# Optimization experiments

Hardware: AMD Instinct MI355X
Metric: run time of the kernel (lower is better)

Reference implementation:

```python
import jax, jax.numpy as jnp
import numpy as np

N = 100000       # nodes
E = 1600000      # edges
NFEAT = 128
NHID = 128
NCLASS = 64
NHEAD = 4
NLAYER = 3
LRELU_ALPHA = 0.2


def setup_inputs() -> dict:
    key = jax.random.key(0)
    ks = jax.random.split(key, 7)
    x = jax.random.normal(ks[0], (N, NFEAT), jnp.float32)
    edge_index = jax.random.randint(ks[1], (2, E), 0, N, jnp.int32)
    # xavier-uniform-ish init scales (gain for relu baked into scale roughly)
    Win = jax.random.normal(ks[2], (NFEAT, NHID), jnp.float32) * (2.0 / (NFEAT + NHID)) ** 0.5
    b_in = jnp.zeros((NHID,), jnp.float32)
    # per hidden layer, per head: a split into (src, dst) halves of the (1, 2*in) vector
    a_hid = jax.random.normal(ks[3], (NLAYER - 1, NHEAD, 2, NHID), jnp.float32) * 0.1
    W_hid = jax.random.normal(ks[4], (NLAYER - 1, NHEAD, NHID, NHID // NHEAD), jnp.float32) * (2.0 / (NHID + NHID // NHEAD)) ** 0.5
    a_out = jax.random.normal(ks[5], (2, NHID), jnp.float32) * 0.1
    W_out = jax.random.normal(ks[6], (NHID, NCLASS), jnp.float32) * (2.0 / (NHID + NCLASS)) ** 0.5
    return dict(x=x, edge_index=edge_index, Win=Win, b_in=b_in,
                a_hid=a_hid, W_hid=W_hid, a_out=a_out, W_out=W_out)


def _segment_softmax(logits, seg, n):
    # numerically stable softmax over groups defined by seg (axis 0)
    m = jax.ops.segment_max(logits, seg, num_segments=n)
    e = jnp.exp(logits - m[seg])
    s = jax.ops.segment_sum(e, seg, num_segments=n)
    return e / s[seg]


def _gat_conv(h, row, col, a, W):
    # h: [N, D]; a: [H, 2, D]; W: [H, D, Dh]
    n = h.shape[0]
    H = a.shape[0]
    s_src = h @ a[:, 0, :].T  # [N, H]
    s_dst = h @ a[:, 1, :].T  # [N, H]
    logits = jax.nn.leaky_relu(s_src[row] + s_dst[col], LRELU_ALPHA)  # [E, H]
    alpha = _segment_softmax(logits, row, n)  # softmax grouped by row (edge_index[0])
    h_col = h[col]  # [E, D] gathered once, reused per head
    outs = []
    for hd in range(H):  # small fixed head loop keeps peak memory at [E, D]
        agg = jax.ops.segment_sum(alpha[:, hd, None] * h_col, row, num_segments=n)  # [N, D]
        outs.append(agg @ W[hd])  # weight applied AFTER aggregation, as in source
    return jnp.concatenate(outs, axis=1)


def reference(x, edge_index, Win, b_in, a_hid, W_hid, a_out, W_out):
    row, col = edge_index[0], edge_index[1]
    h = jax.nn.elu(x @ Win + b_in)  # in_linear + ELU (dropout is identity in eval/p=0)
    for l in range(a_hid.shape[0]):
        h = jax.nn.elu(_gat_conv(h, row, col, a_hid[l], W_hid[l]))
    # final conv: single head to nclass, no activation
    return _gat_conv(h, row, col, a_out[None], W_out[None])
```

## Files before the change

kernel.cpp:

```cpp
#include <hip/hip_runtime.h>
#include <hip/hip_bf16.h>
#include <cstdint>
#include <cstddef>

#define LRELU_ALPHA 0.2f
#define LOG2E 1.44269504088896f

typedef __attribute__((ext_vector_type(8))) short short8;
typedef __attribute__((ext_vector_type(4))) float f32x4;
typedef _Float16 h2v __attribute__((ext_vector_type(2)));

__device__ __forceinline__ unsigned short f2bf(float f) {
    unsigned int u = __float_as_uint(f);
    unsigned int r = (u + 0x7fffu + ((u >> 16) & 1u)) >> 16;
    return (unsigned short)r;
}
__device__ __forceinline__ float bf2f(unsigned int lo16) {
    return __uint_as_float(lo16 << 16);
}
__device__ __forceinline__ unsigned int pk2(float a, float b) {
    return (unsigned int)f2bf(a) | ((unsigned int)f2bf(b) << 16);
}
__device__ __forceinline__ float fexp2(float x) {
#if __has_builtin(__builtin_amdgcn_exp2f)
    return __builtin_amdgcn_exp2f(x);
#else
    return __expf(x * 0.69314718056f);
#endif
}
__device__ __forceinline__ h2v pkrtz(float a, float b) {
#if __has_builtin(__builtin_amdgcn_cvt_pkrtz)
    auto r = __builtin_amdgcn_cvt_pkrtz(a, b);
    union { decltype(r) i; h2v o; } u;
    u.i = r;
    return u.o;
#else
    h2v r; r.x = (_Float16)a; r.y = (_Float16)b; return r;
#endif
}
__device__ __forceinline__ unsigned int pack_lo(unsigned int a, unsigned int b) {
#if __has_builtin(__builtin_amdgcn_perm)
    return __builtin_amdgcn_perm(a, b, 0x01000504u);
#else
    return (a & 0xffffu) | (b << 16);
#endif
}
__device__ __forceinline__ unsigned int pack_hi(unsigned int a, unsigned int b) {
#if __has_builtin(__builtin_amdgcn_perm)
    return __builtin_amdgcn_perm(a, b, 0x03020706u);
#else
    return (a >> 16) | (b & 0xffff0000u);
#endif
}
union U32H2 { unsigned int u; h2v h; };
__device__ __forceinline__ float dot2f(unsigned int a, h2v w, float acc) {
    U32H2 c; c.u = a;
#if __has_builtin(__builtin_amdgcn_fdot2)
    return __builtin_amdgcn_fdot2(c.h, w, acc, false);
#else
    return acc + (float)c.h.x * (float)w.x + (float)c.h.y * (float)w.y;
#endif
}


__global__ void hist8_k(const int* __restrict__ ei, int* __restrict__ counts8,
                        int* __restrict__ rank,
                        float* __restrict__ sdA, float* __restrict__ sdB,
                        float* __restrict__ sdC, unsigned int* __restrict__ hW,
                        int N_, int E_) {
    int rep = blockIdx.x & 7;
    int base = (blockIdx.x * 256 + threadIdx.x) * 8;
    int* cnt = counts8 + (size_t)rep * N_;
    if (base + 8 <= E_) {
        int4 a = *(const int4*)&ei[base];
        int4 b = *(const int4*)&ei[base + 4];
        int rk[8];
        rk[0] = atomicAdd(&cnt[a.x], 1);
        rk[1] = atomicAdd(&cnt[a.y], 1);
        rk[2] = atomicAdd(&cnt[a.z], 1);
        rk[3] = atomicAdd(&cnt[a.w], 1);
        rk[4] = atomicAdd(&cnt[b.x], 1);
        rk[5] = atomicAdd(&cnt[b.y], 1);
        rk[6] = atomicAdd(&cnt[b.z], 1);
        rk[7] = atomicAdd(&cnt[b.w], 1);
        *(int4*)&rank[base]     = make_int4(rk[0], rk[1], rk[2], rk[3]);
        *(int4*)&rank[base + 4] = make_int4(rk[4], rk[5], rk[6], rk[7]);
    } else if (base < E_) {
        for (int j = 0; j < 8 && base + j < E_; j++)
            rank[base + j] = atomicAdd(&cnt[ei[base + j]], 1);
    }
    if (blockIdx.x == 0) {
        int t = threadIdx.x;
        if (t < 4) { sdA[N_ * 4 + t] = -1e30f; sdB[N_ * 4 + t] = -1e30f; }
        if (t == 4) sdC[N_] = -1e30f;
        if (t >= 32 && t < 64)  hW[(size_t)N_ * 32 + (t - 32)] = 0u;
        if (t >= 64 && t < 128) hW[(size_t)N_ * 64 + (t - 64)] = 0u;
    }
}

__global__ void scan_block_k(const int* __restrict__ counts8, int* __restrict__ tmp,
                             int* __restrict__ bsum, int n) {
    __shared__ int s[256];
    int i = blockIdx.x * 256 + threadIdx.x;
    int v = 0;
    if (i < n) {
        int c = 0;
        #pragma unroll
        for (int r = 0; r < 8; r++) c += counts8[(size_t)r * n + i];
        v = (c + 7) & ~7;
    }
    s[threadIdx.x] = v;
    __syncthreads();
    for (int d = 1; d < 256; d <<= 1) {
        int t_ = (threadIdx.x >= d) ? s[threadIdx.x - d] : 0;
        __syncthreads();
        s[threadIdx.x] += t_;
        __syncthreads();
    }
    if (i < n) tmp[i] = s[threadIdx.x];
    if (threadIdx.x == 255) bsum[blockIdx.x] = s[255];
}

__global__ void scan_sums_k(int* bsum, int nb) {
    __shared__ int s[512];
    int v = ((int)threadIdx.x < nb) ? bsum[threadIdx.x] : 0;
    s[threadIdx.x] = v;
    __syncthreads();
    for (int d = 1; d < 512; d <<= 1) {
        int t_ = ((int)threadIdx.x >= d) ? s[threadIdx.x - d] : 0;
        __syncthreads();
        s[threadIdx.x] += t_;
        __syncthreads();
    }
    if ((int)threadIdx.x < nb) bsum[threadIdx.x] = s[threadIdx.x] - v;
}

__global__ void finalize_k(const int* __restrict__ tmp, const int* __restrict__ bsum,
                           const int* __restrict__ counts8, int* __restrict__ base8,
                           int* __restrict__ off, int* __restrict__ scol, int N_, int n) {
    int i = blockIdx.x * 256 + threadIdx.x;
    if (i < n) {
        int end = tmp[i] + bsum[blockIdx.x];
        off[i + 1] = end;
        int c[8], cnt = 0;
        #pragma unroll
        for (int r = 0; r < 8; r++) { c[r] = counts8[(size_t)r * n + i]; cnt += c[r]; }
        int padded = (cnt + 7) & ~7;
        int pos = end - padded;
        #pragma unroll
        for (int r = 0; r < 8; r++) { base8[(size_t)r * n + i] = pos; pos += c[r]; }
        for (; pos < end; pos++) scol[pos] = N_;
    }
    if (i == 0) off[0] = 0;
}

__global__ void scatter8_k(const int* __restrict__ ei, const int* __restrict__ rank,
                           const int* __restrict__ base8, int* __restrict__ scol,
                           int N_, int E_) {
    int rep = blockIdx.x & 7;
    int base = (blockIdx.x * 256 + threadIdx.x) * 8;
    const int* cb = base8 + (size_t)rep * N_;
    if (base + 8 <= E_) {
        int4 a   = *(const int4*)&ei[base];
        int4 b   = *(const int4*)&ei[base + 4];
        int4 ra  = *(const int4*)&rank[base];
        int4 rb  = *(const int4*)&rank[base + 4];
        int4 ca  = *(const int4*)&ei[E_ + base];
        int4 cb4 = *(const int4*)&ei[E_ + base + 4];
        scol[cb[a.x] + ra.x] = ca.x;
        scol[cb[a.y] + ra.y] = ca.y;
        scol[cb[a.z] + ra.z] = ca.z;
        scol[cb[a.w] + ra.w] = ca.w;
        scol[cb[b.x] + rb.x] = cb4.x;
        scol[cb[b.y] + rb.y] = cb4.y;
        scol[cb[b.z] + rb.z] = cb4.z;
        scol[cb[b.w] + rb.w] = cb4.w;
    } else if (base < E_) {
        for (int j = 0; j < 8 && base + j < E_; j++) {
            int r = ei[base + j];
            scol[cb[r] + rank[base + j]] = ei[E_ + base + j];
        }
    }
}


__global__ void repack_all(const float* __restrict__ Win, const float* __restrict__ Whid,
                           const float* __restrict__ ahid, const float* __restrict__ Wout,
                           const float* __restrict__ aout,
                           unsigned short* __restrict__ W0, unsigned short* __restrict__ W1,
                           unsigned short* __restrict__ W2, unsigned short* __restrict__ W3) {
    int i = blockIdx.x * 256 + threadIdx.x;
    if (i < 16384) {
        int n = i >> 7, k = i & 127;
        W0[i] = f2bf(Win[k * 128 + n]);
    } else if (i < 16384 + 2 * 18432) {
        int j = i - 16384;
        int l = j / 18432;
        int jj = j - l * 18432;
        int n = jj >> 7, k = jj & 127;
        float v;
        if (n < 128) {
            int hd = n >> 5, c = n & 31;
            v = Whid[(size_t)l * 16384 + (hd * 128 + k) * 32 + c];
        } else if (n < 136) {
            int ch = n - 128;
            v = ahid[((size_t)l * 8 + ch) * 128 + k] * LOG2E;
        } else {
            v = 0.f;
        }
        (l ? W2 : W1)[jj] = f2bf(v);
    } else if (i < 16384 + 2 * 18432 + 10240) {
        int j = i - (16384 + 2 * 18432);
        int n = j >> 7, k = j & 127;
        float v;
        if (n < 64)       v = Wout[k * 64 + n];
        else if (n < 66)  v = aout[(n - 64) * 128 + k] * LOG2E;
        else              v = 0.f;
        W3[j] = f2bf(v);
    }
}


template <int KJ, int KJA, bool ELU_ACT, bool BIAS, int OUTM, bool ABF16, int SC_H>
__global__ __launch_bounds__(256) void gemm_mfma(const void* __restrict__ Xv,
                                                 const unsigned short* __restrict__ WT,
                                                 const float* __restrict__ bias,
                                                 void* __restrict__ Yv,
                                                 float* __restrict__ ssn,
                                                 float* __restrict__ sdn, int nRows) {
    constexpr int NT = KJA / 16;
    constexpr int NTS = KJ / 16;
    constexpr int WS = 136;
    __shared__ unsigned short sWT[KJA * WS];
    int t = threadIdx.x;
    for (int i = t; i < KJA * 16; i += 256) {
        int n = i >> 4, k8 = i & 15;
        uint4 v = *(const uint4*)&WT[n * 128 + k8 * 8];
        *(uint4*)&sWT[n * WS + k8 * 8] = v;
    }
    __syncthreads();

    int lane = t & 63;
    int wv = t >> 6;
    int m0 = blockIdx.x * 128 + wv * 32;
    int l16 = lane & 15;
    int q4 = lane >> 4;

    short8 afr[4][2];
    #pragma unroll
    for (int rt = 0; rt < 2; rt++) {
        int row = m0 + rt * 16 + l16;
        bool vr = row < nRows;
        if (ABF16) {
            const unsigned int* xp = (const unsigned int*)Xv + (size_t)row * 64 + q4 * 4;
            #pragma unroll
            for (int kk = 0; kk < 4; kk++) {
                uint4 u = make_uint4(0u, 0u, 0u, 0u);
                if (vr) u = *(const uint4*)(xp + kk * 16);
                afr[kk][rt] = *(short8*)&u;
            }
        } else {
            const float* xp = (const float*)Xv + (size_t)row * 128 + q4 * 8;
            #pragma unroll
            for (int kk = 0; kk < 4; kk++) {
                float4 a0 = make_float4(0.f, 0.f, 0.f, 0.f), a1 = a0;
                if (vr) {
                    a0 = *(const float4*)(xp + kk * 32);
                    a1 = *(const float4*)(xp + kk * 32 + 4);
                }
                unsigned int u[4];
                u[0] = pk2(a0.x, a0.y); u[1] = pk2(a0.z, a0.w);
                u[2] = pk2(a1.x, a1.y); u[3] = pk2(a1.z, a1.w);
                afr[kk][rt] = *(short8*)u;
            }
        }
    }

    f32x4 acc[2][NT] = {};
    #pragma unroll
    for (int kk = 0; kk < 4; kk++) {
        #pragma unroll
        for (int ct = 0; ct < NT; ct++) {
            int n = ct * 16 + l16;
            short8 bf = *(const short8*)&sWT[n * WS + kk * 32 + q4 * 8];
            #pragma unroll
            for (int rt = 0; rt < 2; rt++)
                acc[rt][ct] = __builtin_amdgcn_mfma_f32_16x16x32_bf16(afr[kk][rt], bf, acc[rt][ct], 0, 0, 0);
        }
    }

    #pragma unroll
    for (int rt = 0; rt < 2; rt++) {
        #pragma unroll
        for (int q = 0; q < 4; q++) {
            int row = m0 + rt * 16 + q4 * 4 + q;
            if (row >= nRows) continue;
            #pragma unroll
            for (int ct = 0; ct < NTS; ct++) {
                int colc = ct * 16 + l16;
                float v = acc[rt][ct][q];
                if (BIAS) v += bias[colc];
                if (ELU_ACT) v = v > 0.f ? v : (__expf(v) - 1.f);
                if (OUTM == 1) {
                    ((unsigned short*)Yv)[(size_t)row * KJ + colc] = f2bf(v);
                } else if (OUTM == 2) {
                    union { _Float16 hf; unsigned short us; } cv;
                    cv.hf = (_Float16)v;
                    ((unsigned short*)Yv)[(size_t)row * KJ + colc] = cv.us;
                } else {
                    ((float*)Yv)[(size_t)row * KJ + colc] = v;
                }
            }
            if (SC_H > 0) {
                if (l16 < 2 * SC_H) {
                    float v = acc[rt][NT - 1][q];
                    float* dst = (l16 & 1) ? sdn : ssn;
                    dst[row * SC_H + (l16 >> 1)] = v;
                }
            }
        }
    }
}


template <int DHT, int H, bool ELU_ACT, bool BF16O>
__global__ __launch_bounds__(256) void edge_agg_v(const unsigned int* __restrict__ hW2,
                                                  const float* __restrict__ ssrc,
                                                  const float* __restrict__ sdst,
                                                  const int* __restrict__ off,
                                                  const int* __restrict__ scol,
                                                  void* __restrict__ outv, int nRows) {
    constexpr int FPL = DHT / 16;
    constexpr int UPL = FPL / 2;
    int lane = threadIdx.x & 63;
    int sub = lane & 15;
    int g = lane >> 4;
    int wv = threadIdx.x >> 6;
    int r = __builtin_amdgcn_readfirstlane(blockIdx.x * 4 + wv);
    if (r >= nRows) return;
    int begin = off[r], end = off[r + 1];

    int head = (H == 4) ? (sub >> 2) : 0;
    float ssl = ssrc[r * H + head];

    float acc[FPL] = {};
    float den = 0.f;

    for (int i = begin; i < end; i += 8) {
        int2 cc = *(const int2*)&scol[i + 2 * g];
        int cA = cc.x, cB = cc.y;
        float sdA = sdst[cA * H + head];
        float sdB = sdst[cB * H + head];
        unsigned int hA[UPL], hB[UPL];
        int oA = cA * (DHT / 2) + sub * UPL;
        int oB = cB * (DHT / 2) + sub * UPL;
        if (UPL == 4) {
            *(uint4*)hA = *(const uint4*)&hW2[oA];
            *(uint4*)hB = *(const uint4*)&hW2[oB];
        } else {
            *(uint2*)hA = *(const uint2*)&hW2[oA];
            *(uint2*)hB = *(const uint2*)&hW2[oB];
        }
        float lgA = ssl + sdA;
        float wA = fexp2(fmaxf(lgA, LRELU_ALPHA * lgA));
        float lgB = ssl + sdB;
        float wB = fexp2(fmaxf(lgB, LRELU_ALPHA * lgB));
        den += wA + wB;
        h2v w2 = pkrtz(wA, wB);
        #pragma unroll
        for (int q = 0; q < UPL; q++) {
            acc[2 * q]     = dot2f(pack_lo(hA[q], hB[q]), w2, acc[2 * q]);
            acc[2 * q + 1] = dot2f(pack_hi(hA[q], hB[q]), w2, acc[2 * q + 1]);
        }
    }

    #pragma unroll
    for (int s = 16; s < 64; s <<= 1) {
        den += __shfl_xor(den, s);
        #pragma unroll
        for (int p = 0; p < FPL; p++) acc[p] += __shfl_xor(acc[p], s);
    }
    float inv = den > 0.f ? 1.f / den : 0.f;

    float v[FPL];
    #pragma unroll
    for (int p = 0; p < FPL; p++) {
        float tv = acc[p] * inv;
        if (ELU_ACT) tv = tv > 0.f ? tv : (__expf(tv) - 1.f);
        v[p] = tv;
    }

    if (DHT == 128) {
        if (BF16O)
            ((unsigned int*)outv)[(size_t)r * 64 + sub * 4 + g] = pk2(v[2 * g], v[2 * g + 1]);
        else
            *(float2*)&((float*)outv)[(size_t)r * 128 + sub * 8 + 2 * g] =
                make_float2(v[2 * g], v[2 * g + 1]);
    } else {
        ((float*)outv)[(size_t)r * DHT + sub * FPL + g] = v[g];
    }
}


extern "C" void kernel_launch(void* const* d_in, const int* in_sizes, int n_in,
                              void* d_out, int out_size, void* d_ws, size_t ws_size,
                              hipStream_t stream) {
    const float* x    = (const float*)d_in[0];
    const int*   ei   = (const int*)d_in[1];
    const float* Win  = (const float*)d_in[2];
    const float* bin  = (const float*)d_in[3];
    const float* ahid = (const float*)d_in[4];
    const float* Whid = (const float*)d_in[5];
    const float* aout = (const float*)d_in[6];
    const float* Wout = (const float*)d_in[7];
    float* out = (float*)d_out;

    const int N_ = in_sizes[0] / 128;
    const int E_ = in_sizes[1] / 2;

    char* p = (char*)d_ws;
    auto alloc = [&](size_t bytes) {
        char* q = p;
        p += (bytes + 511) & ~(size_t)511;
        return q;
    };
    int* counts8 = (int*)alloc((size_t)N_ * 8 * 4);
    int* base8   = (int*)alloc((size_t)N_ * 8 * 4);
    int* rank    = (int*)alloc((size_t)(E_ + 8) * 4);
    int* tmp     = (int*)alloc((size_t)N_ * 4);
    int* off     = (int*)alloc((size_t)(N_ + 1) * 4);
    int* bsum    = (int*)alloc(4096);
    int* scol    = (int*)alloc((size_t)(E_ + 8 * N_ + 64) * 4);
    float* ssrcA = (float*)alloc((size_t)(N_ + 1) * 4 * 4);
    float* sdstA = (float*)alloc((size_t)(N_ + 1) * 4 * 4);
    float* ssrcB = (float*)alloc((size_t)(N_ + 1) * 4 * 4);
    float* sdstB = (float*)alloc((size_t)(N_ + 1) * 4 * 4);
    float* ssrcC = (float*)alloc((size_t)(N_ + 1) * 4);
    float* sdstC = (float*)alloc((size_t)(N_ + 1) * 4);
    unsigned int* hb  = (unsigned int*)alloc((size_t)N_ * 64 * 4);
    unsigned int* hWb = (unsigned int*)alloc((size_t)(N_ + 1) * 64 * 4);
    unsigned short* WT0 = (unsigned short*)alloc(128 * 128 * 2);
    unsigned short* WT1 = (unsigned short*)alloc(144 * 128 * 2);
    unsigned short* WT2 = (unsigned short*)alloc(144 * 128 * 2);
    unsigned short* WT3 = (unsigned short*)alloc(80 * 128 * 2);

    int NB  = (N_ + 255) / 256;
    int EB8 = (E_ + 2047) / 2048;
    int RT  = (N_ + 127) / 128;
    int NW  = (N_ + 3) / 4;

    (void)hipMemsetAsync(counts8, 0, (size_t)N_ * 8 * 4, stream);
    hist8_k<<<EB8, 256, 0, stream>>>(ei, counts8, rank, sdstA, sdstB, sdstC, hWb, N_, E_);
    scan_block_k<<<NB, 256, 0, stream>>>(counts8, tmp, bsum, N_);
    scan_sums_k<<<1, 512, 0, stream>>>(bsum, NB);
    finalize_k<<<NB, 256, 0, stream>>>(tmp, bsum, counts8, base8, off, scol, N_, N_);
    scatter8_k<<<EB8, 256, 0, stream>>>(ei, rank, base8, scol, N_, E_);

    repack_all<<<248, 256, 0, stream>>>(Win, Whid, ahid, Wout, aout, WT0, WT1, WT2, WT3);

    gemm_mfma<128, 128, true, true, 1, false, 0><<<RT, 256, 0, stream>>>(
        x, WT0, bin, hb, nullptr, nullptr, N_);

    gemm_mfma<128, 144, false, false, 2, true, 4><<<RT, 256, 0, stream>>>(
        hb, WT1, nullptr, hWb, ssrcA, sdstA, N_);
    edge_agg_v<128, 4, true, true><<<NW, 256, 0, stream>>>(
        hWb, ssrcA, sdstA, off, scol, hb, N_);

    gemm_mfma<128, 144, false, false, 2, true, 4><<<RT, 256, 0, stream>>>(
        hb, WT2, nullptr, hWb, ssrcB, sdstB, N_);
    edge_agg_v<128, 4, true, true><<<NW, 256, 0, stream>>>(
        hWb, ssrcB, sdstB, off, scol, hb, N_);

    gemm_mfma<64, 80, false, false, 2, true, 1><<<RT, 256, 0, stream>>>(
        hb, WT3, nullptr, hWb, ssrcC, sdstC, N_);
    edge_agg_v<64, 1, false, false><<<NW, 256, 0, stream>>>(
        hWb, ssrcC, sdstC, off, scol, out, N_);
}
```

Measured before the change: 456.1 us.

## Split 4-head edge aggregation into two half-width blocks per row group

Replaces the hidden-layer edge aggregation kernel with a variant that assigns each wavefront half of the feature columns (two heads), launching twice as many blocks interleaved so both halves of a row group run on adjacent blocks. Each lane loads 8 bytes of features per edge instead of 16 and keeps fewer accumulators, aiming for higher occupancy and more parallelism on the memory-bound gather. The cost is that the CSR column indices and softmax denominators are read and recomputed twice per row.

Measured after the change: 491.7 us. +7.8%, slower.

```diff
diff --git a/kernel.cpp b/kernel.cpp
--- a/kernel.cpp
+++ b/kernel.cpp
@@ -323,6 +323,72 @@
 }
 
 
+template <bool ELU_ACT>
+__global__ __launch_bounds__(256) void edge_agg_half(const unsigned int* __restrict__ hW2,
+                                                     const float* __restrict__ ssrc,
+                                                     const float* __restrict__ sdst,
+                                                     const int* __restrict__ off,
+                                                     const int* __restrict__ scol,
+                                                     unsigned int* __restrict__ outv,
+                                                     int nRowBlk, int nRows) {
+    constexpr int H = 4;
+    int lane = threadIdx.x & 63;
+    int sub = lane & 15;
+    int g = lane >> 4;
+    int wv = threadIdx.x >> 6;
+    int bid = blockIdx.x;
+    int half = (bid & 7) >> 2;
+    int rowblk = (bid >> 3) * 4 + (bid & 3);
+    if (rowblk >= nRowBlk) return;
+    int r = __builtin_amdgcn_readfirstlane(rowblk * 4 + wv);
+    if (r >= nRows) return;
+    int begin = off[r], end = off[r + 1];
+
+    int head = half * 2 + (sub >> 3);
+    float ssl = ssrc[r * H + head];
+    const unsigned int* hWh = hW2 + half * 32 + sub * 2;
+
+    float acc[4] = {};
+    float den = 0.f;
+
+    for (int i = begin; i < end; i += 8) {
+        int2 cc = *(const int2*)&scol[i + 2 * g];
+        int cA = cc.x, cB = cc.y;
+        float sdA = sdst[cA * H + head];
+        float sdB = sdst[cB * H + head];
+        uint2 hA = *(const uint2*)&hWh[cA * 64];
+        uint2 hB = *(const uint2*)&hWh[cB * 64];
+        float lgA = ssl + sdA;
+        float wA = fexp2(fmaxf(lgA, LRELU_ALPHA * lgA));
+        float lgB = ssl + sdB;
+        float wB = fexp2(fmaxf(lgB, LRELU_ALPHA * lgB));
+        den += wA + wB;
+        h2v w2 = pkrtz(wA, wB);
+        acc[0] = dot2f(pack_lo(hA.x, hB.x), w2, acc[0]);
+        acc[1] = dot2f(pack_hi(hA.x, hB.x), w2, acc[1]);
+        acc[2] = dot2f(pack_lo(hA.y, hB.y), w2, acc[2]);
+        acc[3] = dot2f(pack_hi(hA.y, hB.y), w2, acc[3]);
+    }
+
+    #pragma unroll
+    for (int s = 16; s < 64; s <<= 1) {
+        den += __shfl_xor(den, s);
+        #pragma unroll
+        for (int p = 0; p < 4; p++) acc[p] += __shfl_xor(acc[p], s);
+    }
+    float inv = den > 0.f ? 1.f / den : 0.f;
+
+    if (g < 2) {
+        float v0 = acc[2 * g] * inv, v1 = acc[2 * g + 1] * inv;
+        if (ELU_ACT) {
+            v0 = v0 > 0.f ? v0 : (__expf(v0) - 1.f);
+            v1 = v1 > 0.f ? v1 : (__expf(v1) - 1.f);
+        }
+        outv[(size_t)r * 64 + half * 32 + sub * 2 + g] = pk2(v0, v1);
+    }
+}
+
+
 template <int DHT, int H, bool ELU_ACT, bool BF16O>
 __global__ __launch_bounds__(256) void edge_agg_v(const unsigned int* __restrict__ hW2,
                                                   const float* __restrict__ ssrc,
@@ -448,6 +514,7 @@
     int EB8 = (E_ + 2047) / 2048;
     int RT  = (N_ + 127) / 128;
     int NW  = (N_ + 3) / 4;
+    int GH  = 8 * ((NW + 3) / 4);
 
     (void)hipMemsetAsync(counts8, 0, (size_t)N_ * 8 * 4, stream);
     hist8_k<<<EB8, 256, 0, stream>>>(ei, counts8, rank, sdstA, sdstB, sdstC, hWb, N_, E_);
@@ -463,13 +530,13 @@
 
     gemm_mfma<128, 144, false, false, 2, true, 4><<<RT, 256, 0, stream>>>(
         hb, WT1, nullptr, hWb, ssrcA, sdstA, N_);
-    edge_agg_v<128, 4, true, true><<<NW, 256, 0, stream>>>(
-        hWb, ssrcA, sdstA, off, scol, hb, N_);
+    edge_agg_half<true><<<GH, 256, 0, stream>>>(
+        hWb, ssrcA, sdstA, off, scol, hb, NW, N_);
 
     gemm_mfma<128, 144, false, false, 2, true, 4><<<RT, 256, 0, stream>>>(
         hb, WT2, nullptr, hWb, ssrcB, sdstB, N_);
-    edge_agg_v<128, 4, true, true><<<NW, 256, 0, stream>>>(
-        hWb, ssrcB, sdstB, off, scol, hb, N_);
+    edge_agg_half<true><<<GH, 256, 0, stream>>>(
+        hWb, ssrcB, sdstB, off, scol, hb, NW, N_);
 
     gemm_mfma<64, 80, false, false, 2, true, 1><<<RT, 256, 0, stream>>>(
         hb, WT3, nullptr, hWb, ssrcC, sdstC, N_);
```
